# Kernel tuning notes

Hardware: AMD Instinct MI355X
Metric: run time of the kernel (lower is better)

The kernel has to match this reference:

```python
import jax, jax.numpy as jnp
import numpy as np

RADIUS = 1.3
RES = 128
SH_DEG = 2
N_SH = (SH_DEG + 1) ** 2          # 9 SH basis functions
DATA_DIM = N_SH * 3 + 1           # 28: 27 SH rgb coeffs + 1 sigma
STEP = (2.0 * RADIUS / RES) / 2.0 # half a voxel, as in calc_step_size
N_INTRS = int(np.ceil(np.sqrt(3.0) * 2.0 * RES))  # torch.arange(float) length
N_RAYS = 4096


def sh_basis(d):
    # Real spherical harmonics up to degree 2, svox2/plenoxels convention. d: [B,3]
    x, y, z = d[:, 0], d[:, 1], d[:, 2]
    return jnp.stack([
        0.28209479177387814 * jnp.ones_like(x),
        -0.4886025119029199 * y,
        0.4886025119029199 * z,
        -0.4886025119029199 * x,
        1.0925484305920792 * x * y,
        -1.0925484305920792 * y * z,
        0.31539156525252005 * (2.0 * z * z - x * x - y * y),
        -1.0925484305920792 * x * z,
        0.5462742152960396 * (x * x - y * y),
    ], axis=-1)  # [B, 9]


def trilerp(grid, pts):
    # grid: [C, R, R, R] laid out (D,H,W); pts: [N,3] as (x,y,z) in [-1,1],
    # x indexes W, y indexes H, z indexes D (torch grid_sample convention),
    # align_corners=True, padding_mode='border'. Returns [C, N].
    R = grid.shape[-1]
    c = jnp.clip((pts + 1.0) * 0.5 * (R - 1), 0.0, R - 1)  # border padding
    c0 = jnp.floor(c)
    f = c - c0
    i0 = c0.astype(jnp.int32)
    i1 = jnp.minimum(i0 + 1, R - 1)
    x0, y0, z0 = i0[:, 0], i0[:, 1], i0[:, 2]
    x1, y1, z1 = i1[:, 0], i1[:, 1], i1[:, 2]
    fx, fy, fz = f[:, 0], f[:, 1], f[:, 2]
    g = lambda zi, yi, xi: grid[:, zi, yi, xi]  # [C, N]
    out = (g(z0, y0, x0) * ((1 - fz) * (1 - fy) * (1 - fx)) +
           g(z0, y0, x1) * ((1 - fz) * (1 - fy) * fx) +
           g(z0, y1, x0) * ((1 - fz) * fy * (1 - fx)) +
           g(z0, y1, x1) * ((1 - fz) * fy * fx) +
           g(z1, y0, x0) * (fz * (1 - fy) * (1 - fx)) +
           g(z1, y0, x1) * (fz * (1 - fy) * fx) +
           g(z1, y1, x0) * (fz * fy * (1 - fx)) +
           g(z1, y1, x1) * (fz * fy * fx))
    return out


def setup_inputs() -> dict:
    key = jax.random.key(0)
    k1, k2, k3 = jax.random.split(key, 3)
    rays_o = jax.random.normal(k1, (N_RAYS, 3), jnp.float32) * 0.3  # inside cube
    rd = jax.random.normal(k2, (N_RAYS, 3), jnp.float32)
    rays_d = rd / jnp.linalg.norm(rd, axis=-1, keepdims=True)
    # grid parameter: SH coeffs init 0.1, sigma init 0.01 (as in module) + noise
    base = jnp.concatenate([
        jnp.full((1, DATA_DIM - 1, RES, RES, RES), 0.1, jnp.float32),
        jnp.full((1, 1, RES, RES, RES), 0.01, jnp.float32)], axis=1)
    data = base + 0.01 * jax.random.normal(k3, (1, DATA_DIM, RES, RES, RES), jnp.float32)
    return {"rays_o": rays_o, "rays_d": rays_d, "data": data}


def reference(rays_o, rays_d, data):
    # --- ray/box intersection sampling (no grad in original) ---
    ro = jax.lax.stop_gradient(rays_o)
    rd = jax.lax.stop_gradient(rays_d)
    off_pos = (RADIUS - ro) / rd
    off_neg = (-RADIUS - ro) / rd
    start = jnp.max(jnp.minimum(off_pos, off_neg), axis=-1, keepdims=True)  # [B,1]
    steps = jnp.arange(N_INTRS, dtype=ro.dtype)[None, :]
    intersections = start + steps * STEP          # [B, N_INTRS]
    t = intersections[:, :-1]                     # [B, NI]
    pts = ro[:, None, :] + t[..., None] * rd[:, None, :]  # [B, NI, 3]
    mask = jnp.all((pts > -RADIUS) & (pts < RADIUS), axis=-1)  # [B, NI]
    ptsn = pts / RADIUS
    B, NI = t.shape

    # --- trilinear interpolation of grid at all sample points ---
    interp = trilerp(data[0], ptsn.reshape(-1, 3)).T  # [B*NI, 28]
    sigma = jax.nn.relu(interp[:, -1].reshape(B, NI))
    sigma = jnp.where(mask, sigma, 0.0)  # masked_scatter into zeros

    # --- sigma2alpha: standard volumetric compositing weights ---
    dists = (intersections[:, 1:] - intersections[:, :-1]) \
            * jnp.linalg.norm(rays_d, axis=-1, keepdims=True)  # [B, NI]
    alpha = 1.0 - jnp.exp(-sigma * dists)
    trans = jnp.cumprod(jnp.concatenate(
        [jnp.ones((B, 1), alpha.dtype), 1.0 - alpha + 1e-10], axis=1), axis=1)[:, :-1]
    abs_light = alpha * trans  # [B, NI]

    # --- SH -> rgb per sample ---
    sh_mult = sh_basis(rays_d)  # [B, 9]
    sh = interp[:, :-1].reshape(B, NI, 3, N_SH)
    rgb_pts = jnp.einsum('bk,bnck->bnc', sh_mult, sh)  # [B, NI, 3]
    rgb_pts = jnp.where(mask[..., None], rgb_pts, 0.0)  # masked_scatter

    # --- shrgb2rgb: sigmoid, composite, white background ---
    rgb = jnp.sum(abs_light[..., None] * jax.nn.sigmoid(rgb_pts), axis=1)  # [B,3]
    rgb = rgb + (1.0 - jnp.sum(abs_light, axis=1))[..., None]  # white bkgd
    return rgb
```

## Files before the change

kernel.cpp:

```cpp
#include <hip/hip_runtime.h>
#include <math.h>


typedef _Float16 h8 __attribute__((ext_vector_type(8)));

namespace {
constexpr float kRadius   = 1.3f;
constexpr int   kRes      = 128;
constexpr float kStep     = 2.0f * 1.3f / 128.0f / 2.0f;
constexpr int   kNI       = 443;
constexpr int   kNRays    = 4096;
constexpr int   kChStride = kRes * kRes * kRes;
constexpr int   kCh       = 28;
constexpr int   kVoxPad   = 32;
constexpr size_t kVoxBytes = (size_t)kChStride * kVoxPad * sizeof(_Float16);
constexpr int   kChunks4  = 4;
constexpr int   kChunks7  = 7;
}

__global__ __launch_bounds__(256)
void convert_grid(const float* __restrict__ grid, _Float16* __restrict__ vox)
{
    const int v = blockIdx.x * 256 + threadIdx.x;
    h8 o[4];
    #pragma unroll
    for (int c = 0; c < kCh; ++c)
        o[c >> 3][c & 7] = (_Float16)__builtin_nontemporal_load(grid + (size_t)c * kChStride + v);
    o[3][4] = o[3][5] = o[3][6] = o[3][7] = (_Float16)0.f;

    h8* dst = (h8*)(vox + (size_t)v * kVoxPad);
    dst[0] = o[0]; dst[1] = o[1]; dst[2] = o[2]; dst[3] = o[3];
}

struct Sample {
    float alpha;
    float a;
    float rp0, rp1, rp2;
    bool  inb;
};

__device__ __forceinline__ Sample eval_sample(
    int k, float start, float ox, float oy, float oz,
    float dx, float dy, float dz, float dist,
    const float* __restrict__ shm, const _Float16* __restrict__ vox)
{
    Sample s;
    s.alpha = 0.f; s.a = 1.f; s.rp0 = s.rp1 = s.rp2 = 0.f; s.inb = false;
    if (k >= kNI) return s;

    const float t  = start + (float)k * kStep;
    const float px = ox + t*dx;
    const float py = oy + t*dy;
    const float pz = oz + t*dz;
    s.inb = (px > -kRadius) && (px < kRadius) &&
            (py > -kRadius) && (py < kRadius) &&
            (pz > -kRadius) && (pz < kRadius);

    float sig = 0.0f;
    if (s.inb) {
        const float cx = fminf(fmaxf((px*(1.0f/kRadius) + 1.0f)*0.5f*127.0f, 0.0f), 127.0f);
        const float cy = fminf(fmaxf((py*(1.0f/kRadius) + 1.0f)*0.5f*127.0f, 0.0f), 127.0f);
        const float cz = fminf(fmaxf((pz*(1.0f/kRadius) + 1.0f)*0.5f*127.0f, 0.0f), 127.0f);
        const float fx0 = floorf(cx), fy0 = floorf(cy), fz0 = floorf(cz);
        const float fx = cx - fx0, fy = cy - fy0, fz = cz - fz0;
        const int ix0 = (int)fx0, iy0 = (int)fy0, iz0 = (int)fz0;
        const int ix1 = min(ix0 + 1, 127);
        const int iy1 = min(iy0 + 1, 127);
        const int iz1 = min(iz0 + 1, 127);

        const float gx0 = 1.0f - fx, gy0 = 1.0f - fy, gz0 = 1.0f - fz;

        const int offs[8] = {
            iz0*(kRes*kRes) + iy0*kRes + ix0,
            iz0*(kRes*kRes) + iy0*kRes + ix1,
            iz0*(kRes*kRes) + iy1*kRes + ix0,
            iz0*(kRes*kRes) + iy1*kRes + ix1,
            iz1*(kRes*kRes) + iy0*kRes + ix0,
            iz1*(kRes*kRes) + iy0*kRes + ix1,
            iz1*(kRes*kRes) + iy1*kRes + ix0,
            iz1*(kRes*kRes) + iy1*kRes + ix1 };
        const float cw[8] = {
            gz0*gy0*gx0, gz0*gy0*fx, gz0*fy*gx0, gz0*fy*fx,
            fz *gy0*gx0, fz *gy0*fx, fz *fy*gx0, fz *fy*fx };

        #pragma unroll
        for (int cn = 0; cn < 8; ++cn) {
            const h8* vp = (const h8*)(vox + (size_t)offs[cn] * kVoxPad);
            const h8 q0 = vp[0], q1 = vp[1], q2 = vp[2], q3 = vp[3];

            float f[28];
            #pragma unroll
            for (int i = 0; i < 8; ++i) f[i]      = (float)q0[i];
            #pragma unroll
            for (int i = 0; i < 8; ++i) f[8 + i]  = (float)q1[i];
            #pragma unroll
            for (int i = 0; i < 8; ++i) f[16 + i] = (float)q2[i];
            #pragma unroll
            for (int i = 0; i < 4; ++i) f[24 + i] = (float)q3[i];

            float r = 0.f, g = 0.f, b = 0.f;
            #pragma unroll
            for (int j = 0; j < 9; ++j) {
                r = fmaf(shm[j], f[j],      r);
                g = fmaf(shm[j], f[9 + j],  g);
                b = fmaf(shm[j], f[18 + j], b);
            }
            const float wc = cw[cn];
            s.rp0 = fmaf(wc, r, s.rp0);
            s.rp1 = fmaf(wc, g, s.rp1);
            s.rp2 = fmaf(wc, b, s.rp2);
            sig   = fmaf(wc, f[27], sig);
        }
        sig = fmaxf(sig, 0.0f);
    }
    s.alpha = 1.0f - expf(-sig * dist);
    s.a     = 1.0f - s.alpha + 1e-10f;
    return s;
}

__global__ __launch_bounds__(256, 3)
void render_chunks(const float* __restrict__ rays_o,
                   const float* __restrict__ rays_d,
                   const _Float16* __restrict__ vox,
                   float* __restrict__ partials)
{
    const int lane  = threadIdx.x & 63;
    const int W     = blockIdx.x * 4 + (threadIdx.x >> 6);
    const int ray   = W >> 2;
    const int chunk = W & 3;

    const float ox = rays_o[3*ray+0], oy = rays_o[3*ray+1], oz = rays_o[3*ray+2];
    const float dx = rays_d[3*ray+0], dy = rays_d[3*ray+1], dz = rays_d[3*ray+2];

    const float sx = fminf(( kRadius - ox)/dx, (-kRadius - ox)/dx);
    const float sy = fminf(( kRadius - oy)/dy, (-kRadius - oy)/dy);
    const float sz = fminf(( kRadius - oz)/dz, (-kRadius - oz)/dz);
    const float start = fmaxf(sx, fmaxf(sy, sz));
    const float dnorm = sqrtf(dx*dx + dy*dy + dz*dz);
    const float dist  = kStep * dnorm;

    float shm[9];
    shm[0] =  0.28209479177387814f;
    shm[1] = -0.4886025119029199f * dy;
    shm[2] =  0.4886025119029199f * dz;
    shm[3] = -0.4886025119029199f * dx;
    shm[4] =  1.0925484305920792f * dx * dy;
    shm[5] = -1.0925484305920792f * dy * dz;
    shm[6] =  0.31539156525252005f * (2.0f*dz*dz - dx*dx - dy*dy);
    shm[7] = -1.0925484305920792f * dx * dz;
    shm[8] =  0.5462742152960396f * (dx*dx - dy*dy);

    const int base = chunk * 128;
    const Sample A = eval_sample(base + lane,      start, ox, oy, oz, dx, dy, dz, dist, shm, vox);
    const Sample B = eval_sample(base + 64 + lane, start, ox, oy, oz, dx, dy, dz, dist, shm, vox);

    float prodA = A.a;
    #pragma unroll
    for (int off = 1; off < 64; off <<= 1) {
        const float y = __shfl_up(prodA, off, 64);
        if (lane >= off) prodA *= y;
    }
    float exclA = __shfl_up(prodA, 1, 64);
    if (lane == 0) exclA = 1.0f;
    const float P0 = __shfl(prodA, 63, 64);

    float prodB = B.a;
    #pragma unroll
    for (int off = 1; off < 64; off <<= 1) {
        const float y = __shfl_up(prodB, off, 64);
        if (lane >= off) prodB *= y;
    }
    float exclB = __shfl_up(prodB, 1, 64);
    if (lane == 0) exclB = 1.0f;
    const float P1 = __shfl(prodB, 63, 64);

    const float wA = A.alpha * exclA;
    const float wB = B.alpha * P0 * exclB;

    float sR = 0.f, sG = 0.f, sB = 0.f;
    if (A.inb) {
        sR = wA * (1.0f / (1.0f + expf(-A.rp0)));
        sG = wA * (1.0f / (1.0f + expf(-A.rp1)));
        sB = wA * (1.0f / (1.0f + expf(-A.rp2)));
    }
    if (B.inb) {
        sR = fmaf(wB, 1.0f / (1.0f + expf(-B.rp0)), sR);
        sG = fmaf(wB, 1.0f / (1.0f + expf(-B.rp1)), sG);
        sB = fmaf(wB, 1.0f / (1.0f + expf(-B.rp2)), sB);
    }
    float sL = wA + wB;
    const float P = P0 * P1;

    #pragma unroll
    for (int off = 32; off > 0; off >>= 1) {
        sR += __shfl_down(sR, off, 64);
        sG += __shfl_down(sG, off, 64);
        sB += __shfl_down(sB, off, 64);
        sL += __shfl_down(sL, off, 64);
    }

    if (lane == 0) {
        float* p = partials + (size_t)(ray * kChunks4 + chunk) * 5;
        p[0] = sR; p[1] = sG; p[2] = sB; p[3] = sL; p[4] = P;
    }
}

__global__ __launch_bounds__(256)
void combine_chunks(const float* __restrict__ partials, float* __restrict__ out)
{
    const int r = blockIdx.x * 256 + threadIdx.x;
    const float* p = partials + (size_t)r * (kChunks4 * 5);

    float carry = 1.0f, aR = 0.f, aG = 0.f, aB = 0.f, aL = 0.f;
    #pragma unroll
    for (int c = 0; c < kChunks4; ++c) {
        aR = fmaf(carry, p[c*5 + 0], aR);
        aG = fmaf(carry, p[c*5 + 1], aG);
        aB = fmaf(carry, p[c*5 + 2], aB);
        aL = fmaf(carry, p[c*5 + 3], aL);
        carry *= p[c*5 + 4];
    }
    const float bg = 1.0f - aL;
    out[3*r + 0] = aR + bg;
    out[3*r + 1] = aG + bg;
    out[3*r + 2] = aB + bg;
}

#define TRI8(p) (w000*(p)[o000] + w001*(p)[o001] + w010*(p)[o010] + w011*(p)[o011] \
               + w100*(p)[o100] + w101*(p)[o101] + w110*(p)[o110] + w111*(p)[o111])

__global__ __launch_bounds__(256)
void plenoxel_render_direct(const float* __restrict__ rays_o,
                            const float* __restrict__ rays_d,
                            const float* __restrict__ grid,
                            float* __restrict__ out)
{
    const int lane = threadIdx.x & 63;
    const int ray  = blockIdx.x * 4 + (threadIdx.x >> 6);

    const float ox = rays_o[3*ray+0], oy = rays_o[3*ray+1], oz = rays_o[3*ray+2];
    const float dx = rays_d[3*ray+0], dy = rays_d[3*ray+1], dz = rays_d[3*ray+2];

    const float sx = fminf(( kRadius - ox)/dx, (-kRadius - ox)/dx);
    const float sy = fminf(( kRadius - oy)/dy, (-kRadius - oy)/dy);
    const float sz = fminf(( kRadius - oz)/dz, (-kRadius - oz)/dz);
    const float start = fmaxf(sx, fmaxf(sy, sz));
    const float dnorm = sqrtf(dx*dx + dy*dy + dz*dz);

    float shm[9];
    shm[0] =  0.28209479177387814f;
    shm[1] = -0.4886025119029199f * dy;
    shm[2] =  0.4886025119029199f * dz;
    shm[3] = -0.4886025119029199f * dx;
    shm[4] =  1.0925484305920792f * dx * dy;
    shm[5] = -1.0925484305920792f * dy * dz;
    shm[6] =  0.31539156525252005f * (2.0f*dz*dz - dx*dx - dy*dy);
    shm[7] = -1.0925484305920792f * dx * dz;
    shm[8] =  0.5462742152960396f * (dx*dx - dy*dy);

    float carry = 1.0f;
    float accR = 0.f, accG = 0.f, accB = 0.f, accL = 0.f;

    for (int chunk = 0; chunk < kChunks7; ++chunk) {
        const int k = chunk * 64 + lane;
        float alpha = 0.0f, a = 1.0f;
        float rp0 = 0.f, rp1 = 0.f, rp2 = 0.f;
        bool inb = false;

        if (k < kNI) {
            const float t = start + (float)k * kStep;
            const float dist = kStep * dnorm;
            const float px = ox + t*dx, py = oy + t*dy, pz = oz + t*dz;
            inb = (px > -kRadius) && (px < kRadius) &&
                  (py > -kRadius) && (py < kRadius) &&
                  (pz > -kRadius) && (pz < kRadius);
            float sigma = 0.0f;
            if (inb) {
                const float cx = fminf(fmaxf((px*(1.0f/kRadius) + 1.0f)*0.5f*127.0f, 0.0f), 127.0f);
                const float cy = fminf(fmaxf((py*(1.0f/kRadius) + 1.0f)*0.5f*127.0f, 0.0f), 127.0f);
                const float cz = fminf(fmaxf((pz*(1.0f/kRadius) + 1.0f)*0.5f*127.0f, 0.0f), 127.0f);
                const float fx0 = floorf(cx), fy0 = floorf(cy), fz0 = floorf(cz);
                const float fx = cx - fx0, fy = cy - fy0, fz = cz - fz0;
                const int ix0 = (int)fx0, iy0 = (int)fy0, iz0 = (int)fz0;
                const int ix1 = min(ix0 + 1, 127);
                const int iy1 = min(iy0 + 1, 127);
                const int iz1 = min(iz0 + 1, 127);
                const float gx0 = 1.0f - fx, gy0 = 1.0f - fy, gz0 = 1.0f - fz;
                const float w000 = gz0*gy0*gx0, w001 = gz0*gy0*fx;
                const float w010 = gz0*fy *gx0, w011 = gz0*fy *fx;
                const float w100 = fz *gy0*gx0, w101 = fz *gy0*fx;
                const float w110 = fz *fy *gx0, w111 = fz *fy *fx;
                const int o000 = iz0*(kRes*kRes) + iy0*kRes + ix0;
                const int o001 = iz0*(kRes*kRes) + iy0*kRes + ix1;
                const int o010 = iz0*(kRes*kRes) + iy1*kRes + ix0;
                const int o011 = iz0*(kRes*kRes) + iy1*kRes + ix1;
                const int o100 = iz1*(kRes*kRes) + iy0*kRes + ix0;
                const int o101 = iz1*(kRes*kRes) + iy0*kRes + ix1;
                const int o110 = iz1*(kRes*kRes) + iy1*kRes + ix0;
                const int o111 = iz1*(kRes*kRes) + iy1*kRes + ix1;
                #pragma unroll
                for (int kk = 0; kk < 9; ++kk) {
                    rp0 = fmaf(shm[kk], TRI8(grid + (kk     ) * kChStride), rp0);
                    rp1 = fmaf(shm[kk], TRI8(grid + (kk +  9) * kChStride), rp1);
                    rp2 = fmaf(shm[kk], TRI8(grid + (kk + 18) * kChStride), rp2);
                }
                sigma = fmaxf(TRI8(grid + 27 * kChStride), 0.0f);
            }
            alpha = 1.0f - expf(-sigma * dist);
            a     = 1.0f - alpha + 1e-10f;
        }

        float prod = a;
        #pragma unroll
        for (int off = 1; off < 64; off <<= 1) {
            const float y = __shfl_up(prod, off, 64);
            if (lane >= off) prod *= y;
        }
        float excl = __shfl_up(prod, 1, 64);
        if (lane == 0) excl = 1.0f;
        const float trans = carry * excl;
        const float w = alpha * trans;
        if (inb) {
            accR = fmaf(w, 1.0f / (1.0f + expf(-rp0)), accR);
            accG = fmaf(w, 1.0f / (1.0f + expf(-rp1)), accG);
            accB = fmaf(w, 1.0f / (1.0f + expf(-rp2)), accB);
        }
        accL += w;
        carry *= __shfl(prod, 63, 64);
    }

    #pragma unroll
    for (int off = 32; off > 0; off >>= 1) {
        accR += __shfl_down(accR, off, 64);
        accG += __shfl_down(accG, off, 64);
        accB += __shfl_down(accB, off, 64);
        accL += __shfl_down(accL, off, 64);
    }

    if (lane == 0) {
        const float bg = 1.0f - accL;
        out[3*ray + 0] = accR + bg;
        out[3*ray + 1] = accG + bg;
        out[3*ray + 2] = accB + bg;
    }
}

extern "C" void kernel_launch(void* const* d_in, const int* in_sizes, int n_in,
                              void* d_out, int out_size, void* d_ws, size_t ws_size,
                              hipStream_t stream) {
    const float* rays_o = (const float*)d_in[0];
    const float* rays_d = (const float*)d_in[1];
    const float* data   = (const float*)d_in[2];
    float* out = (float*)d_out;

    const size_t partBytes = (size_t)kNRays * kChunks4 * 5 * sizeof(float);
    const size_t need = kVoxBytes + partBytes;

    if (ws_size >= need) {
        _Float16* vox = (_Float16*)d_ws;
        float* partials = (float*)((char*)d_ws + kVoxBytes);

        hipLaunchKernelGGL(convert_grid,
                           dim3(kChStride / 256), dim3(256), 0, stream,
                           data, vox);
        hipLaunchKernelGGL(render_chunks,
                           dim3(kNRays * kChunks4 / 4), dim3(256), 0, stream,
                           rays_o, rays_d, vox, partials);
        hipLaunchKernelGGL(combine_chunks,
                           dim3(kNRays / 256), dim3(256), 0, stream,
                           partials, out);
    } else {
        hipLaunchKernelGGL(plenoxel_render_direct,
                           dim3(kNRays / 4), dim3(256), 0, stream,
                           rays_o, rays_d, data, out);
    }
}
```

Measured before the change: 403.6 us.

## Use two 256-sample chunks per ray and skip chunks past the cube exit

Each ray is now split into two wavefront chunks of four 64-sample groups each, instead of four chunks of two groups. A chunk whose first sample lies beyond the ray's exit from the bounding cube returns early and writes an identity partial. Those samples were all out of bounds and contributed nothing, so skipping them avoids their evaluation and scans. The trade-off is more live registers per wave, fewer waves overall, and per-ray load imbalance.

```diff
diff --git a/kernel.cpp b/kernel.cpp
--- a/kernel.cpp
+++ b/kernel.cpp
@@ -14,7 +14,7 @@
 constexpr int   kCh       = 28;
 constexpr int   kVoxPad   = 32;
 constexpr size_t kVoxBytes = (size_t)kChStride * kVoxPad * sizeof(_Float16);
-constexpr int   kChunks4  = 4;
+constexpr int   kChunks   = 2;
 constexpr int   kChunks7  = 7;
 }
 
@@ -118,6 +118,20 @@
     return s;
 }
 
+__device__ __forceinline__ float wave_scan_prod(float a, int lane, float& total)
+{
+    float prod = a;
+    #pragma unroll
+    for (int off = 1; off < 64; off <<= 1) {
+        const float y = __shfl_up(prod, off, 64);
+        if (lane >= off) prod *= y;
+    }
+    float excl = __shfl_up(prod, 1, 64);
+    if (lane == 0) excl = 1.0f;
+    total = __shfl(prod, 63, 64);
+    return excl;
+}
+
 __global__ __launch_bounds__(256, 3)
 void render_chunks(const float* __restrict__ rays_o,
                    const float* __restrict__ rays_d,
@@ -126,16 +140,28 @@
 {
     const int lane  = threadIdx.x & 63;
     const int W     = blockIdx.x * 4 + (threadIdx.x >> 6);
-    const int ray   = W >> 2;
-    const int chunk = W & 3;
+    const int ray   = W >> 1;
+    const int chunk = W & 1;
 
     const float ox = rays_o[3*ray+0], oy = rays_o[3*ray+1], oz = rays_o[3*ray+2];
     const float dx = rays_d[3*ray+0], dy = rays_d[3*ray+1], dz = rays_d[3*ray+2];
 
-    const float sx = fminf(( kRadius - ox)/dx, (-kRadius - ox)/dx);
-    const float sy = fminf(( kRadius - oy)/dy, (-kRadius - oy)/dy);
-    const float sz = fminf(( kRadius - oz)/dz, (-kRadius - oz)/dz);
-    const float start = fmaxf(sx, fmaxf(sy, sz));
+    const float ppx = ( kRadius - ox)/dx, pnx = (-kRadius - ox)/dx;
+    const float ppy = ( kRadius - oy)/dy, pny = (-kRadius - oy)/dy;
+    const float ppz = ( kRadius - oz)/dz, pnz = (-kRadius - oz)/dz;
+    const float start  = fmaxf(fminf(ppx, pnx), fmaxf(fminf(ppy, pny), fminf(ppz, pnz)));
+    const float t_exit = fminf(fmaxf(ppx, pnx), fminf(fmaxf(ppy, pny), fmaxf(ppz, pnz)));
+
+    const int base = chunk * 256;
+
+    if (start + (float)base * kStep > t_exit + kStep) {
+        if (lane == 0) {
+            float* p = partials + (size_t)(ray * kChunks + chunk) * 5;
+            p[0] = 0.f; p[1] = 0.f; p[2] = 0.f; p[3] = 0.f; p[4] = 1.f;
+        }
+        return;
+    }
+
     const float dnorm = sqrtf(dx*dx + dy*dy + dz*dz);
     const float dist  = kStep * dnorm;
 
@@ -150,32 +176,21 @@
     shm[7] = -1.0925484305920792f * dx * dz;
     shm[8] =  0.5462742152960396f * (dx*dx - dy*dy);
 
-    const int base = chunk * 128;
-    const Sample A = eval_sample(base + lane,      start, ox, oy, oz, dx, dy, dz, dist, shm, vox);
-    const Sample B = eval_sample(base + 64 + lane, start, ox, oy, oz, dx, dy, dz, dist, shm, vox);
-
-    float prodA = A.a;
-    #pragma unroll
-    for (int off = 1; off < 64; off <<= 1) {
-        const float y = __shfl_up(prodA, off, 64);
-        if (lane >= off) prodA *= y;
-    }
-    float exclA = __shfl_up(prodA, 1, 64);
-    if (lane == 0) exclA = 1.0f;
-    const float P0 = __shfl(prodA, 63, 64);
-
-    float prodB = B.a;
-    #pragma unroll
-    for (int off = 1; off < 64; off <<= 1) {
-        const float y = __shfl_up(prodB, off, 64);
-        if (lane >= off) prodB *= y;
-    }
-    float exclB = __shfl_up(prodB, 1, 64);
-    if (lane == 0) exclB = 1.0f;
-    const float P1 = __shfl(prodB, 63, 64);
-
-    const float wA = A.alpha * exclA;
-    const float wB = B.alpha * P0 * exclB;
+    const Sample A = eval_sample(base       + lane, start, ox, oy, oz, dx, dy, dz, dist, shm, vox);
+    const Sample B = eval_sample(base +  64 + lane, start, ox, oy, oz, dx, dy, dz, dist, shm, vox);
+    const Sample C = eval_sample(base + 128 + lane, start, ox, oy, oz, dx, dy, dz, dist, shm, vox);
+    const Sample D = eval_sample(base + 192 + lane, start, ox, oy, oz, dx, dy, dz, dist, shm, vox);
+
+    float P0, P1, P2, P3;
+    const float eA = wave_scan_prod(A.a, lane, P0);
+    const float eB = wave_scan_prod(B.a, lane, P1);
+    const float eC = wave_scan_prod(C.a, lane, P2);
+    const float eD = wave_scan_prod(D.a, lane, P3);
+
+    const float wA = A.alpha * eA;
+    const float wB = B.alpha * P0 * eB;
+    const float wC = C.alpha * P0 * P1 * eC;
+    const float wD = D.alpha * P0 * P1 * P2 * eD;
 
     float sR = 0.f, sG = 0.f, sB = 0.f;
     if (A.inb) {
@@ -188,8 +203,18 @@
         sG = fmaf(wB, 1.0f / (1.0f + expf(-B.rp1)), sG);
         sB = fmaf(wB, 1.0f / (1.0f + expf(-B.rp2)), sB);
     }
-    float sL = wA + wB;
-    const float P = P0 * P1;
+    if (C.inb) {
+        sR = fmaf(wC, 1.0f / (1.0f + expf(-C.rp0)), sR);
+        sG = fmaf(wC, 1.0f / (1.0f + expf(-C.rp1)), sG);
+        sB = fmaf(wC, 1.0f / (1.0f + expf(-C.rp2)), sB);
+    }
+    if (D.inb) {
+        sR = fmaf(wD, 1.0f / (1.0f + expf(-D.rp0)), sR);
+        sG = fmaf(wD, 1.0f / (1.0f + expf(-D.rp1)), sG);
+        sB = fmaf(wD, 1.0f / (1.0f + expf(-D.rp2)), sB);
+    }
+    float sL = wA + wB + wC + wD;
+    const float P = P0 * P1 * P2 * P3;
 
     #pragma unroll
     for (int off = 32; off > 0; off >>= 1) {
@@ -200,7 +225,7 @@
     }
 
     if (lane == 0) {
-        float* p = partials + (size_t)(ray * kChunks4 + chunk) * 5;
+        float* p = partials + (size_t)(ray * kChunks + chunk) * 5;
         p[0] = sR; p[1] = sG; p[2] = sB; p[3] = sL; p[4] = P;
     }
 }
@@ -209,11 +234,11 @@
 void combine_chunks(const float* __restrict__ partials, float* __restrict__ out)
 {
     const int r = blockIdx.x * 256 + threadIdx.x;
-    const float* p = partials + (size_t)r * (kChunks4 * 5);
+    const float* p = partials + (size_t)r * (kChunks * 5);
 
     float carry = 1.0f, aR = 0.f, aG = 0.f, aB = 0.f, aL = 0.f;
     #pragma unroll
-    for (int c = 0; c < kChunks4; ++c) {
+    for (int c = 0; c < kChunks; ++c) {
         aR = fmaf(carry, p[c*5 + 0], aR);
         aG = fmaf(carry, p[c*5 + 1], aG);
         aB = fmaf(carry, p[c*5 + 2], aB);
@@ -353,7 +378,7 @@
     const float* data   = (const float*)d_in[2];
     float* out = (float*)d_out;
 
-    const size_t partBytes = (size_t)kNRays * kChunks4 * 5 * sizeof(float);
+    const size_t partBytes = (size_t)kNRays * kChunks * 5 * sizeof(float);
     const size_t need = kVoxBytes + partBytes;
 
     if (ws_size >= need) {
@@ -364,7 +389,7 @@
                            dim3(kChStride / 256), dim3(256), 0, stream,
                            data, vox);
         hipLaunchKernelGGL(render_chunks,
-                           dim3(kNRays * kChunks4 / 4), dim3(256), 0, stream,
+                           dim3(kNRays * kChunks / 4), dim3(256), 0, stream,
                            rays_o, rays_d, vox, partials);
         hipLaunchKernelGGL(combine_chunks,
                            dim3(kNRays / 256), dim3(256), 0, stream,
```

Result: faster. 393.7 us (-2.4%).
